# Kernel optimization log

Hardware: AMD Instinct MI355X
Metric: run time of the kernel (lower is better)

Reference implementation:

```python
import jax, jax.numpy as jnp
import numpy as np

B, NTH, NTW, M, DF = 64, 56, 56, 8, 8
FAR = 100.0  # sentinel location for off sources, as in the torch module


def setup_inputs() -> dict:
    key = jax.random.key(0)
    k1, k2, k3, k4, k5 = jax.random.split(key, 5)
    est_locs = jax.random.uniform(k1, (B, NTH, NTW, M, 2), dtype=jnp.float32)
    true_locs = jax.random.uniform(k2, (B, NTH, NTW, M, 2), dtype=jnp.float32)
    true_fluxes = jax.random.normal(k3, (B, NTH, NTW, M, DF), dtype=jnp.float32)
    est_n_sources = jax.random.randint(k4, (B, NTH, NTW), 0, M + 1, dtype=jnp.int32)
    true_n_sources = jax.random.randint(k5, (B, NTH, NTW), 0, M + 1, dtype=jnp.int32)
    return {"est_locs": est_locs, "true_locs": true_locs, "true_fluxes": true_fluxes,
            "est_n_sources": est_n_sources, "true_n_sources": true_n_sources}


def reference(est_locs, true_locs, true_fluxes, est_n_sources, true_n_sources):
    b, nth, ntw, m, _ = est_locs.shape
    T = b * nth * ntw
    slot = jnp.arange(m)
    # is_on_mask per tile: first n_sources slots are on
    est_on = slot[None, :] < est_n_sources.reshape(T, 1)    # [T, m] bool
    true_on = slot[None, :] < true_n_sources.reshape(T, 1)  # [T, m] bool

    # masked locs -> pairwise L2 distances (torch.cdist p=2)
    el = jnp.where(est_on[..., None], est_locs.reshape(T, m, 2), jnp.float32(FAR))
    tl = jnp.where(true_on[..., None], true_locs.reshape(T, m, 2), jnp.float32(FAR))
    diff = el[:, :, None, :] - tl[:, None, :, :]
    dist = jnp.sqrt(jnp.sum(diff * diff, axis=-1))  # [T, m, m]

    # _fast_one_to_one_match
    match1 = jnp.argmin(dist, axis=1)  # best est row per true col  [T, m]
    match2 = jnp.argmin(dist, axis=2)  # best true col per est row  [T, m]
    match1cond2 = jnp.take_along_axis(match1, match2, axis=1)
    one2one = match1cond2 == slot[None, :]
    est_out = match1 > (est_on.sum(-1, keepdims=True) - 1)
    true_out = match2 > (true_on.sum(-1, keepdims=True) - 1)
    one2one = one2one & ~(est_out | true_out)
    # unmatched pairs point to the padded dump slot m (== est_to_true*mask + offset)
    est_idx = jnp.where(one2one, match1, m)
    true_idx = jnp.where(one2one, match2, m)

    # flat indices across (b*nth*ntw) tiles, each of width m+1
    tile_off = (jnp.arange(T) * (m + 1))[:, None]
    flat_est = (est_idx + tile_off).reshape(-1)
    flat_true = (true_idx + tile_off).reshape(-1)

    # padded true catalog: locs(2) | fluxes(DF) | n_sources-indicator(1)
    fields = jnp.concatenate([
        true_locs.reshape(T, m, 2),
        true_fluxes.reshape(T, m, -1),
        true_on[..., None].astype(jnp.float32),
    ], axis=-1)  # [T, m, 2+DF+1]
    d = fields.shape[-1]
    padded = jnp.concatenate([fields, jnp.zeros((T, 1, d), fields.dtype)], axis=1)
    padded = padded.reshape(T * (m + 1), d)

    # gather matched true rows, scatter into est positions (zeros init)
    target = jnp.zeros_like(padded).at[flat_est].set(padded[flat_true])
    target = target.reshape(T, m + 1, d)[:, :m]  # drop dump slot (v[..., :-1, :])
    return target.reshape(b, nth, ntw, m, d)
```

## Files before the change

### kernel.cpp

```cpp
#include <hip/hip_runtime.h>
#include <math.h>

constexpr int TT = 64 * 56 * 56;
__global__ __launch_bounds__(64) void mvd_fused_dense64(
    const float4* __restrict__ el4,
    const float4* __restrict__ tl4,
    const float*  __restrict__ tf,
    const int*    __restrict__ en_,
    const int*    __restrict__ tn_,
    float4*       __restrict__ out4)
{
#pragma clang fp contract(off)
    const int t0 = blockIdx.x * 64;
    const int t  = t0 + threadIdx.x;

    __shared__ int s_rowsrc[64];

    {
        const int en = en_[t];
        const int tn = tn_[t];

        float4 ea = el4[t * 4 + 0], eb = el4[t * 4 + 1];
        float4 ec = el4[t * 4 + 2], ed = el4[t * 4 + 3];
        float4 ta = tl4[t * 4 + 0], tb = tl4[t * 4 + 1];
        float4 tc = tl4[t * 4 + 2], td = tl4[t * 4 + 3];

        float mex[8], mey[8], mtx[8], mty[8];
        {
            const float exs[8] = {ea.x, ea.z, eb.x, eb.z, ec.x, ec.z, ed.x, ed.z};
            const float eys[8] = {ea.y, ea.w, eb.y, eb.w, ec.y, ec.w, ed.y, ed.w};
            const float txs[8] = {ta.x, ta.z, tb.x, tb.z, tc.x, tc.z, td.x, td.z};
            const float tys[8] = {ta.y, ta.w, tb.y, tb.w, tc.y, tc.w, td.y, td.w};
#pragma unroll
            for (int i = 0; i < 8; i++) {
                mex[i] = (i < en) ? exs[i] : 100.0f;
                mey[i] = (i < en) ? eys[i] : 100.0f;
                mtx[i] = (i < tn) ? txs[i] : 100.0f;
                mty[i] = (i < tn) ? tys[i] : 100.0f;
            }
        }

        float colmin[8];
        int   m1[8], m2[8];
#pragma unroll
        for (int j = 0; j < 8; j++) { colmin[j] = 1e30f; m1[j] = 0; }
#pragma unroll
        for (int i = 0; i < 8; i++) {
            float rmin = 1e30f;
            int   rj = 0;
#pragma unroll
            for (int j = 0; j < 8; j++) {
                float dx = mex[i] - mtx[j];
                float dy = mey[i] - mty[j];
                float dx2 = dx * dx;
                float dy2 = dy * dy;
                float d = sqrtf(dx2 + dy2);
                if (d < rmin) { rmin = d; rj = j; }
                if (d < colmin[j]) { colmin[j] = d; m1[j] = i; }
            }
            m2[i] = rj;
        }

        int m1p = 0;
#pragma unroll
        for (int j = 0; j < 8; j++) m1p |= m1[j] << (3 * j);

        int rowsrc = 0;
#pragma unroll
        for (int k = 0; k < 8; k++) {
            int j = m2[k];
            int m1j = (m1p >> (3 * j)) & 7;
            bool o2o = (m1j == k) && (m1[k] < en) && (m2[k] < tn);
            if (o2o) {
                int r = m1[k];
                rowsrc = (rowsrc & ~(0xF << (4 * r))) | ((8 | j) << (4 * r));
            }
        }
        s_rowsrc[threadIdx.x] = rowsrc;
    }
    __syncthreads();

    const float* tl = (const float*)tl4;
    float4* oblk = out4 + (size_t)t0 * 22;

#pragma unroll
    for (int it = 0; it < 22; it++) {
        const int i   = threadIdx.x + it * 64;
        const int tl_ = i / 22;
        const int q   = i - tl_ * 22;
        const int w   = s_rowsrc[tl_];
        const int tt  = t0 + tl_;

        float res[4];
#pragma unroll
        for (int u = 0; u < 4; u++) {
            int p = 4 * q + u;
            int r = (p * 94) >> 10;
            int c = p - r * 11;
            int v = (w >> (4 * r)) & 15;
            float val = 0.0f;
            if (v & 8) {
                int j = v & 7;
                if (c == 10)      val = 1.0f;
                else if (c < 2)   val = tl[(tt << 4) + (j << 1) + c];
                else              val = tf[(tt << 6) + (j << 3) + (c - 2)];
            }
            res[u] = val;
        }
        oblk[i] = make_float4(res[0], res[1], res[2], res[3]);
    }
}

extern "C" void kernel_launch(void* const* d_in, const int* in_sizes, int n_in,
                              void* d_out, int out_size, void* d_ws, size_t ws_size,
                              hipStream_t stream) {
    const float* est_locs    = (const float*)d_in[0];
    const float* true_locs   = (const float*)d_in[1];
    const float* true_fluxes = (const float*)d_in[2];
    const int*   est_n       = (const int*)d_in[3];
    const int*   true_n      = (const int*)d_in[4];
    float* out = (float*)d_out;

    mvd_fused_dense64<<<TT / 64, 64, 0, stream>>>(
        (const float4*)est_locs, (const float4*)true_locs, true_fluxes,
        est_n, true_n, (float4*)out);
}
```

Measured before the change: 150.8 us.

## Stage true locs and fluxes in LDS and gather matched rows from shared memory

Each block now loads its 64 tiles of true locations and fluxes into LDS with coalesced float4 loads before the matching step. The output phase then reads matched rows from LDS instead of doing scattered scalar global gathers. The per-tile match word is passed with a wavefront shuffle rather than through a shared array, and the divide by 22 becomes a multiply-shift. The cost is about 20KB of LDS per 64-thread block, which may limit occupancy, plus loading all fluxes even for unmatched slots.

```diff
diff --git a/kernel.cpp b/kernel.cpp
--- a/kernel.cpp
+++ b/kernel.cpp
@@ -2,20 +2,32 @@
 #include <math.h>
 
 constexpr int TT = 64 * 56 * 56;
-__global__ __launch_bounds__(64) void mvd_fused_dense64(
+__global__ __launch_bounds__(64) void mvd_lds_gather(
     const float4* __restrict__ el4,
     const float4* __restrict__ tl4,
-    const float*  __restrict__ tf,
+    const float4* __restrict__ tf4,
     const int*    __restrict__ en_,
     const int*    __restrict__ tn_,
     float4*       __restrict__ out4)
 {
 #pragma clang fp contract(off)
-    const int t0 = blockIdx.x * 64;
-    const int t  = t0 + threadIdx.x;
+    const int lane = threadIdx.x;
+    const int t0   = blockIdx.x * 64;
+    const int t    = t0 + lane;
 
-    __shared__ int s_rowsrc[64];
+    __shared__ float s_mem[1024 + 4096];
 
+    {
+        float4* sm4 = (float4*)s_mem;
+#pragma unroll
+        for (int k = 0; k < 4; k++)
+            sm4[k * 64 + lane] = tl4[(size_t)t0 * 4 + k * 64 + lane];
+#pragma unroll
+        for (int k = 0; k < 16; k++)
+            sm4[256 + k * 64 + lane] = tf4[(size_t)t0 * 16 + k * 64 + lane];
+    }
+
+    int rowsrc = 0;
     {
         const int en = en_[t];
         const int tn = tn_[t];
@@ -65,7 +77,6 @@
 #pragma unroll
         for (int j = 0; j < 8; j++) m1p |= m1[j] << (3 * j);
 
-        int rowsrc = 0;
 #pragma unroll
         for (int k = 0; k < 8; k++) {
             int j = m2[k];
@@ -76,20 +87,17 @@
                 rowsrc = (rowsrc & ~(0xF << (4 * r))) | ((8 | j) << (4 * r));
             }
         }
-        s_rowsrc[threadIdx.x] = rowsrc;
     }
     __syncthreads();
 
-    const float* tl = (const float*)tl4;
     float4* oblk = out4 + (size_t)t0 * 22;
 
 #pragma unroll
     for (int it = 0; it < 22; it++) {
-        const int i   = threadIdx.x + it * 64;
-        const int tl_ = i / 22;
+        const int i   = lane + it * 64;
+        const int tl_ = (i * 2979) >> 16;
         const int q   = i - tl_ * 22;
-        const int w   = s_rowsrc[tl_];
-        const int tt  = t0 + tl_;
+        const int w   = __shfl(rowsrc, tl_);
 
         float res[4];
 #pragma unroll
@@ -98,14 +106,13 @@
             int r = (p * 94) >> 10;
             int c = p - r * 11;
             int v = (w >> (4 * r)) & 15;
-            float val = 0.0f;
-            if (v & 8) {
-                int j = v & 7;
-                if (c == 10)      val = 1.0f;
-                else if (c < 2)   val = tl[(tt << 4) + (j << 1) + c];
-                else              val = tf[(tt << 6) + (j << 3) + (c - 2)];
-            }
-            res[u] = val;
+            bool matched = (v & 8) != 0;
+            int  j = v & 7;
+            int a_tl = tl_ * 16 + 2 * j + c;
+            int a_tf = 1024 + tl_ * 64 + 8 * j + (c-2);
+            int addr = (!matched || c >= 10) ? 0 : (c < 2 ? a_tl : a_tf);
+            float val = s_mem[addr];
+            res[u] = matched ? (c == 10 ? 1.0f : val) : 0.0f;
         }
         oblk[i] = make_float4(res[0], res[1], res[2], res[3]);
     }
@@ -121,7 +128,7 @@
     const int*   true_n      = (const int*)d_in[4];
     float* out = (float*)d_out;
 
-    mvd_fused_dense64<<<TT / 64, 64, 0, stream>>>(
-        (const float4*)est_locs, (const float4*)true_locs, true_fluxes,
-        est_n, true_n, (float4*)out);
+    mvd_lds_gather<<<TT / 64, 64, 0, stream>>>(
+        (const float4*)est_locs, (const float4*)true_locs,
+        (const float4*)true_fluxes, est_n, true_n, (float4*)out);
 }
```

Result: no change. 149.2 us (-1.1%).

## Split fused kernel into match kernel and flat branchless output-writer kernel

Applied to the files above, without the earlier changes.

The fused kernel is split in two. The first kernel computes the one-to-one match per tile and stores a packed row-source word in workspace. The second kernel uses 256-thread blocks, one thread per output float4, and gathers with branchless loads, always reading an in-bounds address and selecting the value afterwards. The aim is better occupancy and more memory parallelism in the write phase, at the cost of a second launch, a workspace round trip, and reads that are done even for unmatched rows.

```diff
diff --git a/kernel.cpp b/kernel.cpp
--- a/kernel.cpp
+++ b/kernel.cpp
@@ -2,113 +2,109 @@
 #include <math.h>
 
 constexpr int TT = 64 * 56 * 56;
-__global__ __launch_bounds__(64) void mvd_fused_dense64(
+
+__global__ __launch_bounds__(64) void mvd_match_only(
     const float4* __restrict__ el4,
     const float4* __restrict__ tl4,
-    const float*  __restrict__ tf,
     const int*    __restrict__ en_,
     const int*    __restrict__ tn_,
+    int*          __restrict__ match)
+{
+#pragma clang fp contract(off)
+    const int t = blockIdx.x * 64 + threadIdx.x;
+
+    const int en = en_[t];
+    const int tn = tn_[t];
+
+    float4 ea = el4[t * 4 + 0], eb = el4[t * 4 + 1];
+    float4 ec = el4[t * 4 + 2], ed = el4[t * 4 + 3];
+    float4 ta = tl4[t * 4 + 0], tb = tl4[t * 4 + 1];
+    float4 tc = tl4[t * 4 + 2], td = tl4[t * 4 + 3];
+
+    float mex[8], mey[8], mtx[8], mty[8];
+    {
+        const float exs[8] = {ea.x, ea.z, eb.x, eb.z, ec.x, ec.z, ed.x, ed.z};
+        const float eys[8] = {ea.y, ea.w, eb.y, eb.w, ec.y, ec.w, ed.y, ed.w};
+        const float txs[8] = {ta.x, ta.z, tb.x, tb.z, tc.x, tc.z, td.x, td.z};
+        const float tys[8] = {ta.y, ta.w, tb.y, tb.w, tc.y, tc.w, td.y, td.w};
+#pragma unroll
+        for (int i = 0; i < 8; i++) {
+            mex[i] = (i < en) ? exs[i] : 100.0f;
+            mey[i] = (i < en) ? eys[i] : 100.0f;
+            mtx[i] = (i < tn) ? txs[i] : 100.0f;
+            mty[i] = (i < tn) ? tys[i] : 100.0f;
+        }
+    }
+
+    float colmin[8];
+    int   m1[8], m2[8];
+#pragma unroll
+    for (int j = 0; j < 8; j++) { colmin[j] = 1e30f; m1[j] = 0; }
+#pragma unroll
+    for (int i = 0; i < 8; i++) {
+        float rmin = 1e30f;
+        int   rj = 0;
+#pragma unroll
+        for (int j = 0; j < 8; j++) {
+            float dx = mex[i] - mtx[j];
+            float dy = mey[i] - mty[j];
+            float dx2 = dx * dx;
+            float dy2 = dy * dy;
+            float d = sqrtf(dx2 + dy2);
+            if (d < rmin) { rmin = d; rj = j; }
+            if (d < colmin[j]) { colmin[j] = d; m1[j] = i; }
+        }
+        m2[i] = rj;
+    }
+
+    int m1p = 0;
+#pragma unroll
+    for (int j = 0; j < 8; j++) m1p |= m1[j] << (3 * j);
+
+    int rowsrc = 0;
+#pragma unroll
+    for (int k = 0; k < 8; k++) {
+        int j = m2[k];
+        int m1j = (m1p >> (3 * j)) & 7;
+        bool o2o = (m1j == k) && (m1[k] < en) && (m2[k] < tn);
+        if (o2o) {
+            int r = m1[k];
+            rowsrc = (rowsrc & ~(0xF << (4 * r))) | ((8 | j) << (4 * r));
+        }
+    }
+    match[t] = rowsrc;
+}
+
+__global__ __launch_bounds__(256) void mvd_write_flat(
+    const float*  __restrict__ tl,
+    const float*  __restrict__ tf,
+    const int*    __restrict__ match,
     float4*       __restrict__ out4)
 {
-#pragma clang fp contract(off)
-    const int t0 = blockIdx.x * 64;
-    const int t  = t0 + threadIdx.x;
+    const int idx = blockIdx.x * 256 + threadIdx.x;
+    const int t = idx / 22;
+    const int q = idx - t * 22;
+    const int w = match[t];
 
-    __shared__ int s_rowsrc[64];
+    float res[4];
+#pragma unroll
+    for (int u = 0; u < 4; u++) {
+        const int p = 4 * q + u;
+        const int r = (p * 94) >> 10;
+        const int c = p - r * 11;
+        const int v = (w >> (4 * r)) & 15;
+        const int j = v & 7;
 
-    {
-        const int en = en_[t];
-        const int tn = tn_[t];
+        const float* pa = tl + ((t << 4) + (j << 1) + (c & 1));
+        const int ct = (c > 9) ? 7 : (c - 2);
+        const float* pb = tf + ((t << 6) + (j << 3) + ct);
+        const float* pr = (c < 2) ? pa : pb;
+        const float val = *pr;
 
-        float4 ea = el4[t * 4 + 0], eb = el4[t * 4 + 1];
-        float4 ec = el4[t * 4 + 2], ed = el4[t * 4 + 3];
-        float4 ta = tl4[t * 4 + 0], tb = tl4[t * 4 + 1];
-        float4 tc = tl4[t * 4 + 2], td = tl4[t * 4 + 3];
-
-        float mex[8], mey[8], mtx[8], mty[8];
-        {
-            const float exs[8] = {ea.x, ea.z, eb.x, eb.z, ec.x, ec.z, ed.x, ed.z};
-            const float eys[8] = {ea.y, ea.w, eb.y, eb.w, ec.y, ec.w, ed.y, ed.w};
-            const float txs[8] = {ta.x, ta.z, tb.x, tb.z, tc.x, tc.z, td.x, td.z};
-            const float tys[8] = {ta.y, ta.w, tb.y, tb.w, tc.y, tc.w, td.y, td.w};
-#pragma unroll
-            for (int i = 0; i < 8; i++) {
-                mex[i] = (i < en) ? exs[i] : 100.0f;
-                mey[i] = (i < en) ? eys[i] : 100.0f;
-                mtx[i] = (i < tn) ? txs[i] : 100.0f;
-                mty[i] = (i < tn) ? tys[i] : 100.0f;
-            }
-        }
-
-        float colmin[8];
-        int   m1[8], m2[8];
-#pragma unroll
-        for (int j = 0; j < 8; j++) { colmin[j] = 1e30f; m1[j] = 0; }
-#pragma unroll
-        for (int i = 0; i < 8; i++) {
-            float rmin = 1e30f;
-            int   rj = 0;
-#pragma unroll
-            for (int j = 0; j < 8; j++) {
-                float dx = mex[i] - mtx[j];
-                float dy = mey[i] - mty[j];
-                float dx2 = dx * dx;
-                float dy2 = dy * dy;
-                float d = sqrtf(dx2 + dy2);
-                if (d < rmin) { rmin = d; rj = j; }
-                if (d < colmin[j]) { colmin[j] = d; m1[j] = i; }
-            }
-            m2[i] = rj;
-        }
-
-        int m1p = 0;
-#pragma unroll
-        for (int j = 0; j < 8; j++) m1p |= m1[j] << (3 * j);
-
-        int rowsrc = 0;
-#pragma unroll
-        for (int k = 0; k < 8; k++) {
-            int j = m2[k];
-            int m1j = (m1p >> (3 * j)) & 7;
-            bool o2o = (m1j == k) && (m1[k] < en) && (m2[k] < tn);
-            if (o2o) {
-                int r = m1[k];
-                rowsrc = (rowsrc & ~(0xF << (4 * r))) | ((8 | j) << (4 * r));
-            }
-        }
-        s_rowsrc[threadIdx.x] = rowsrc;
+        const float sel = (c == 10) ? 1.0f : val;
+        res[u] = (v & 8) ? sel : 0.0f;
     }
-    __syncthreads();
-
-    const float* tl = (const float*)tl4;
-    float4* oblk = out4 + (size_t)t0 * 22;
-
-#pragma unroll
-    for (int it = 0; it < 22; it++) {
-        const int i   = threadIdx.x + it * 64;
-        const int tl_ = i / 22;
-        const int q   = i - tl_ * 22;
-        const int w   = s_rowsrc[tl_];
-        const int tt  = t0 + tl_;
-
-        float res[4];
-#pragma unroll
-        for (int u = 0; u < 4; u++) {
-            int p = 4 * q + u;
-            int r = (p * 94) >> 10;
-            int c = p - r * 11;
-            int v = (w >> (4 * r)) & 15;
-            float val = 0.0f;
-            if (v & 8) {
-                int j = v & 7;
-                if (c == 10)      val = 1.0f;
-                else if (c < 2)   val = tl[(tt << 4) + (j << 1) + c];
-                else              val = tf[(tt << 6) + (j << 3) + (c - 2)];
-            }
-            res[u] = val;
-        }
-        oblk[i] = make_float4(res[0], res[1], res[2], res[3]);
-    }
+    out4[idx] = make_float4(res[0], res[1], res[2], res[3]);
 }
 
 extern "C" void kernel_launch(void* const* d_in, const int* in_sizes, int n_in,
@@ -121,7 +117,12 @@
     const int*   true_n      = (const int*)d_in[4];
     float* out = (float*)d_out;
 
-    mvd_fused_dense64<<<TT / 64, 64, 0, stream>>>(
-        (const float4*)est_locs, (const float4*)true_locs, true_fluxes,
-        est_n, true_n, (float4*)out);
+    int* match = (int*)d_ws;
+
+    mvd_match_only<<<TT / 64, 64, 0, stream>>>(
+        (const float4*)est_locs, (const float4*)true_locs,
+        est_n, true_n, match);
+
+    mvd_write_flat<<<(TT * 22) / 256, 256, 0, stream>>>(
+        true_locs, true_fluxes, match, (float4*)out);
 }
```

After: 155.6 us. 1.03x slower.
